# Kernel optimization log

Hardware: AMD Instinct MI355X
Metric: run time of the kernel (lower is better)

## Reference

```python
import jax, jax.numpy as jnp
import numpy as np

B, S, N, F, H, E = 1, 32, 2048, 64, 128, 32768


def setup_inputs() -> dict:
    key = jax.random.key(0)
    ks = jax.random.split(key, 13)
    p = lambda k, shp: (jax.random.normal(k, shp, dtype=jnp.float32) * 0.05)
    return {
        "x": jax.random.normal(ks[0], (B, S, N, F), dtype=jnp.float32),
        "edge_indexs": jax.random.randint(ks[1], (1, 2, S * E), 0, N, dtype=jnp.int64),
        "edgenum": E,
        "W1": p(ks[2], (F, H)), "b1": p(ks[3], (H,)),
        "W2": p(ks[4], (H, H)), "b2": p(ks[5], (H,)),
        "Wrel": p(ks[6], (H, H)), "brel": p(ks[7], (H,)),
        "Wroot": p(ks[8], (H, H)),
        "W3": p(ks[9], (H, H)), "b3": p(ks[10], (H,)),
        "W4": p(ks[11], (H, 1)), "b4": p(ks[12], (1,)),
    }


def reference(x, edge_indexs, edgenum, W1, b1, W2, b2, Wrel, brel, Wroot, W3, b3, W4, b4):
    batch, seq_len, num_stocks, _ = x.shape
    lrelu = jax.nn.leaky_relu  # default slope 0.01, matches nn.LeakyReLU()
    h = lrelu(x @ W1 + b1)
    h = lrelu(h @ W2 + b2)                       # [B,S,N,H]
    h = h.reshape(seq_len, num_stocks, -1)       # batch==1
    # split of [2, S*E] along edge dim into per-timestep graphs
    edges = edge_indexs[0].reshape(2, seq_len, edgenum)

    def step(h_t, src, tgt):
        # GraphConv(aggr='mean'): lin_rel(mean_j x_j) + lin_root(x_i)
        agg = jax.ops.segment_sum(h_t[src], tgt, num_segments=num_stocks)
        cnt = jax.ops.segment_sum(jnp.ones((edgenum,), h_t.dtype), tgt,
                                  num_segments=num_stocks)
        agg = agg / jnp.maximum(cnt, 1.0)[:, None]
        # all gnn layers share weights and each re-reads output[i], so one
        # application reproduces the original loop's final `out` exactly
        return lrelu(agg @ Wrel + brel + h_t @ Wroot)

    gnn_out = jax.vmap(step)(h, edges[0], edges[1])          # [S,N,H]
    out = gnn_out.reshape(batch, seq_len, num_stocks, -1)
    out = lrelu(out @ W3 + b3)
    out = out @ W4 + b4                                      # [B,S,N,1]
    return out[:, -1].reshape(batch, num_stocks, -1)
```

## Files before the change

kernel.cpp:

```cpp
#include <hip/hip_runtime.h>


#define N_NODES 2048
#define F_IN 64
#define H_DIM 128
#define S_LEN 32
#define E_EDGES 32768
#define T_LAST (S_LEN - 1)
#define CAP 96
#define NBLK 256
#define TPB 512

__device__ __forceinline__ float lrelu(float v) { return v > 0.0f ? v : 0.01f * v; }

__global__ __launch_bounds__(TPB) void k_fused(
    const float* __restrict__ x, const int* __restrict__ ei,
    const float* __restrict__ W1, const float* __restrict__ b1,
    const float* __restrict__ W2, const float* __restrict__ b2,
    const float* __restrict__ Wrel, const float* __restrict__ brel,
    const float* __restrict__ Wroot,
    const float* __restrict__ W3, const float* __restrict__ b3,
    const float* __restrict__ W4, const float* __restrict__ b4,
    float* __restrict__ out,
    int* __restrict__ deg, unsigned int* __restrict__ bar,
    int* __restrict__ bucket, float* __restrict__ h2)
{
    __shared__ float xs[8][F_IN];
    __shared__ float h1s[8][H_DIM];
    __shared__ float aggs[8][H_DIM];
    __shared__ float h2s[8][H_DIM];
    __shared__ float gs[8][H_DIM];
    __shared__ int   bl[8][CAP];
    __shared__ int   dgs[8];
    __shared__ float pred[8][2];

    const int t = threadIdx.x;
    const int bid = blockIdx.x;
    const int node0 = bid * 8;

    if (t < 128) {
        const int e = bid * 128 + t;
        const int src = ei[(size_t)T_LAST * E_EDGES + e];
        const int tgt = ei[(size_t)(S_LEN + T_LAST) * E_EDGES + e];
        const int slot = atomicAdd(&deg[tgt], 1);
        if (slot < CAP) bucket[tgt * CAP + slot] = src;
    }

    if (t < 256) {
        const float* xsrc = x + ((size_t)T_LAST * N_NODES + node0) * F_IN;
        ((float2*)&xs[0][0])[t] = ((const float2*)xsrc)[t];
    }
    __syncthreads();

    const int j = t & 127;
    const int q = t >> 7;
    const int nb = q * 2;

    {
        const float bb = b1[j];
        float a0 = bb, a1 = bb;
        for (int k = 0; k < F_IN; ++k) {
            const float w = W1[k * H_DIM + j];
            a0 += xs[nb][k] * w; a1 += xs[nb + 1][k] * w;
        }
        h1s[nb][j] = lrelu(a0); h1s[nb + 1][j] = lrelu(a1);
    }
    __syncthreads();
    {
        const float bb = b2[j];
        float a0 = bb, a1 = bb;
        for (int k = 0; k < H_DIM; ++k) {
            const float w = W2[k * H_DIM + j];
            a0 += h1s[nb][k] * w; a1 += h1s[nb + 1][k] * w;
        }
        a0 = lrelu(a0); a1 = lrelu(a1);
        h2[(size_t)(node0 + nb) * H_DIM + j] = a0;
        h2[(size_t)(node0 + nb + 1) * H_DIM + j] = a1;
        h2s[nb][j] = a0; h2s[nb + 1][j] = a1;
    }

    __syncthreads();
    if (t == 0) {
        __hip_atomic_fetch_add(bar, 1u, __ATOMIC_ACQ_REL, __HIP_MEMORY_SCOPE_AGENT);
        while (__hip_atomic_load(bar, __ATOMIC_ACQUIRE, __HIP_MEMORY_SCOPE_AGENT) < NBLK)
            __builtin_amdgcn_s_sleep(1);
    }
    __syncthreads();

    {
        const int g = t >> 6, lane = t & 63;
        const int n = node0 + g;
        const int dg = min(deg[n], CAP);
        if (lane == 0) dgs[g] = dg;
        for (int i = lane; i < dg; i += 64) bl[g][i] = bucket[n * CAP + i];
    }
    __syncthreads();

    #pragma unroll
    for (int m = 0; m < 2; ++m) {
        const int n = nb + m;
        const int dg = dgs[n];
        float acc = 0.0f;
        for (int i = 0; i < dg; ++i)
            acc += h2[(size_t)bl[n][i] * H_DIM + j];
        aggs[n][j] = acc / fmaxf((float)dg, 1.0f);
    }
    __syncthreads();

    {
        const float bb = brel[j];
        float a0 = bb, a1 = bb;
        for (int k = 0; k < H_DIM; ++k) {
            const float wr = Wrel[k * H_DIM + j];
            const float wo = Wroot[k * H_DIM + j];
            a0 += aggs[nb][k] * wr + h2s[nb][k] * wo;
            a1 += aggs[nb + 1][k] * wr + h2s[nb + 1][k] * wo;
        }
        gs[nb][j] = lrelu(a0); gs[nb + 1][j] = lrelu(a1);
    }
    __syncthreads();

    float p0, p1;
    {
        const float bb = b3[j];
        float a0 = bb, a1 = bb;
        for (int k = 0; k < H_DIM; ++k) {
            const float w = W3[k * H_DIM + j];
            a0 += gs[nb][k] * w; a1 += gs[nb + 1][k] * w;
        }
        const float w4 = W4[j];
        p0 = lrelu(a0) * w4; p1 = lrelu(a1) * w4;
    }
    for (int off = 32; off >= 1; off >>= 1) {
        p0 += __shfl_down(p0, off);
        p1 += __shfl_down(p1, off);
    }
    const int w = t >> 6;
    if ((t & 63) == 0) { pred[w][0] = p0; pred[w][1] = p1; }
    __syncthreads();
    if (t < 8) {
        const int n = t, qq = n >> 1, mm = n & 1;
        out[node0 + n] = pred[2 * qq][mm] + pred[2 * qq + 1][mm] + b4[0];
    }
}

extern "C" void kernel_launch(void* const* d_in, const int* in_sizes, int n_in,
                              void* d_out, int out_size, void* d_ws, size_t ws_size,
                              hipStream_t stream)
{
    const float* x     = (const float*)d_in[0];
    const int*   ei    = (const int*)d_in[1];
    const float* W1    = (const float*)d_in[3];
    const float* b1    = (const float*)d_in[4];
    const float* W2    = (const float*)d_in[5];
    const float* b2    = (const float*)d_in[6];
    const float* Wrel  = (const float*)d_in[7];
    const float* brel  = (const float*)d_in[8];
    const float* Wroot = (const float*)d_in[9];
    const float* W3    = (const float*)d_in[10];
    const float* b3    = (const float*)d_in[11];
    const float* W4    = (const float*)d_in[12];
    const float* b4    = (const float*)d_in[13];
    float* out = (float*)d_out;

    int*      deg    = (int*)d_ws;
    unsigned* bar    = (unsigned*)((int*)d_ws + 2048);
    int*      bucket = (int*)d_ws + 2064;
    float*    h2     = (float*)((int*)d_ws + 2064 + N_NODES * CAP);

    hipMemsetAsync(d_ws, 0, (2048 + 16) * sizeof(int), stream);

    k_fused<<<NBLK, TPB, 0, stream>>>(x, ei, W1, b1, W2, b2, Wrel, brel, Wroot,
                                      W3, b3, W4, b4, out, deg, bar, bucket, h2);
}
```

Baseline: 128.1 us.

## Split fused kernel at grid barrier into two launches with one node per thread-row

Replaces the software grid-wide spin barrier with a kernel boundary, splitting the fused kernel into an MLP/edge-bucketing kernel and a GNN aggregation/head kernel. Block size doubles to 1024 threads so each thread computes one node-feature output instead of two. The neighbour-gather loop is unrolled by four with independent accumulators to expose more memory parallelism. This trades the spin-wait for an extra launch and reloading h2 from global memory, and halves per-thread weight reuse.

After: 161.7 us. +26.2%, slower.

```diff
diff --git a/kernel.cpp b/kernel.cpp
--- a/kernel.cpp
+++ b/kernel.cpp
@@ -9,31 +9,18 @@
 #define T_LAST (S_LEN - 1)
 #define CAP 96
 #define NBLK 256
-#define TPB 512
+#define TPB 1024
 
 __device__ __forceinline__ float lrelu(float v) { return v > 0.0f ? v : 0.01f * v; }
 
-__global__ __launch_bounds__(TPB) void k_fused(
+__global__ __launch_bounds__(TPB) void kA(
     const float* __restrict__ x, const int* __restrict__ ei,
     const float* __restrict__ W1, const float* __restrict__ b1,
     const float* __restrict__ W2, const float* __restrict__ b2,
-    const float* __restrict__ Wrel, const float* __restrict__ brel,
-    const float* __restrict__ Wroot,
-    const float* __restrict__ W3, const float* __restrict__ b3,
-    const float* __restrict__ W4, const float* __restrict__ b4,
-    float* __restrict__ out,
-    int* __restrict__ deg, unsigned int* __restrict__ bar,
-    int* __restrict__ bucket, float* __restrict__ h2)
+    int* __restrict__ deg, int* __restrict__ bucket, float* __restrict__ h2)
 {
     __shared__ float xs[8][F_IN];
     __shared__ float h1s[8][H_DIM];
-    __shared__ float aggs[8][H_DIM];
-    __shared__ float h2s[8][H_DIM];
-    __shared__ float gs[8][H_DIM];
-    __shared__ int   bl[8][CAP];
-    __shared__ int   dgs[8];
-    __shared__ float pred[8][2];
-
     const int t = threadIdx.x;
     const int bid = blockIdx.x;
     const int node0 = bid * 8;
@@ -46,102 +33,82 @@
         if (slot < CAP) bucket[tgt * CAP + slot] = src;
     }
 
-    if (t < 256) {
-        const float* xsrc = x + ((size_t)T_LAST * N_NODES + node0) * F_IN;
-        ((float2*)&xs[0][0])[t] = ((const float2*)xsrc)[t];
-    }
+    if (t < 512)
+        ((float*)xs)[t] = x[((size_t)T_LAST * N_NODES + node0) * F_IN + t];
     __syncthreads();
 
+    const int n = t >> 7;
     const int j = t & 127;
-    const int q = t >> 7;
-    const int nb = q * 2;
 
-    {
-        const float bb = b1[j];
-        float a0 = bb, a1 = bb;
-        for (int k = 0; k < F_IN; ++k) {
-            const float w = W1[k * H_DIM + j];
-            a0 += xs[nb][k] * w; a1 += xs[nb + 1][k] * w;
-        }
-        h1s[nb][j] = lrelu(a0); h1s[nb + 1][j] = lrelu(a1);
-    }
-    __syncthreads();
-    {
-        const float bb = b2[j];
-        float a0 = bb, a1 = bb;
-        for (int k = 0; k < H_DIM; ++k) {
-            const float w = W2[k * H_DIM + j];
-            a0 += h1s[nb][k] * w; a1 += h1s[nb + 1][k] * w;
-        }
-        a0 = lrelu(a0); a1 = lrelu(a1);
-        h2[(size_t)(node0 + nb) * H_DIM + j] = a0;
-        h2[(size_t)(node0 + nb + 1) * H_DIM + j] = a1;
-        h2s[nb][j] = a0; h2s[nb + 1][j] = a1;
-    }
-
-    __syncthreads();
-    if (t == 0) {
-        __hip_atomic_fetch_add(bar, 1u, __ATOMIC_ACQ_REL, __HIP_MEMORY_SCOPE_AGENT);
-        while (__hip_atomic_load(bar, __ATOMIC_ACQUIRE, __HIP_MEMORY_SCOPE_AGENT) < NBLK)
-            __builtin_amdgcn_s_sleep(1);
-    }
+    float acc = b1[j];
+    #pragma unroll
+    for (int k = 0; k < F_IN; ++k)
+        acc += xs[n][k] * W1[k * H_DIM + j];
+    h1s[n][j] = lrelu(acc);
     __syncthreads();
 
-    {
-        const int g = t >> 6, lane = t & 63;
-        const int n = node0 + g;
-        const int dg = min(deg[n], CAP);
-        if (lane == 0) dgs[g] = dg;
-        for (int i = lane; i < dg; i += 64) bl[g][i] = bucket[n * CAP + i];
-    }
+    float a2 = b2[j];
+    #pragma unroll
+    for (int k = 0; k < H_DIM; ++k)
+        a2 += h1s[n][k] * W2[k * H_DIM + j];
+    h2[(size_t)(node0 + n) * H_DIM + j] = lrelu(a2);
+}
+
+__global__ __launch_bounds__(TPB) void kB(
+    const float* __restrict__ h2,
+    const int* __restrict__ deg, const int* __restrict__ bucket,
+    const float* __restrict__ Wrel, const float* __restrict__ brel,
+    const float* __restrict__ Wroot,
+    const float* __restrict__ W3, const float* __restrict__ b3,
+    const float* __restrict__ W4, const float* __restrict__ b4,
+    float* __restrict__ out)
+{
+    __shared__ float h2s[8][H_DIM];
+    __shared__ float aggs[8][H_DIM];
+    __shared__ float gs[8][H_DIM];
+    __shared__ int   bl[8][CAP];
+    __shared__ float pred[16];
+    const int t = threadIdx.x;
+    const int node0 = blockIdx.x * 8;
+    const int n = t >> 7;
+    const int j = t & 127;
+
+    h2s[n][j] = h2[(size_t)(node0 + n) * H_DIM + j];
+    const int dg = min(deg[node0 + n], CAP);
+    if (j < dg) bl[n][j] = bucket[(node0 + n) * CAP + j];
     __syncthreads();
 
-    #pragma unroll
-    for (int m = 0; m < 2; ++m) {
-        const int n = nb + m;
-        const int dg = dgs[n];
-        float acc = 0.0f;
-        for (int i = 0; i < dg; ++i)
-            acc += h2[(size_t)bl[n][i] * H_DIM + j];
-        aggs[n][j] = acc / fmaxf((float)dg, 1.0f);
+    float a0 = 0.f, a1 = 0.f, a2 = 0.f, a3 = 0.f;
+    int i = 0;
+    for (; i + 3 < dg; i += 4) {
+        const int s0 = bl[n][i], s1 = bl[n][i + 1], s2 = bl[n][i + 2], s3 = bl[n][i + 3];
+        a0 += h2[(size_t)s0 * H_DIM + j];
+        a1 += h2[(size_t)s1 * H_DIM + j];
+        a2 += h2[(size_t)s2 * H_DIM + j];
+        a3 += h2[(size_t)s3 * H_DIM + j];
     }
+    for (; i < dg; ++i) a0 += h2[(size_t)bl[n][i] * H_DIM + j];
+    aggs[n][j] = ((a0 + a1) + (a2 + a3)) / fmaxf((float)dg, 1.0f);
     __syncthreads();
 
-    {
-        const float bb = brel[j];
-        float a0 = bb, a1 = bb;
-        for (int k = 0; k < H_DIM; ++k) {
-            const float wr = Wrel[k * H_DIM + j];
-            const float wo = Wroot[k * H_DIM + j];
-            a0 += aggs[nb][k] * wr + h2s[nb][k] * wo;
-            a1 += aggs[nb + 1][k] * wr + h2s[nb + 1][k] * wo;
-        }
-        gs[nb][j] = lrelu(a0); gs[nb + 1][j] = lrelu(a1);
-    }
+    float g = brel[j];
+    #pragma unroll
+    for (int k = 0; k < H_DIM; ++k)
+        g += aggs[n][k] * Wrel[k * H_DIM + j] + h2s[n][k] * Wroot[k * H_DIM + j];
+    gs[n][j] = lrelu(g);
     __syncthreads();
 
-    float p0, p1;
-    {
-        const float bb = b3[j];
-        float a0 = bb, a1 = bb;
-        for (int k = 0; k < H_DIM; ++k) {
-            const float w = W3[k * H_DIM + j];
-            a0 += gs[nb][k] * w; a1 += gs[nb + 1][k] * w;
-        }
-        const float w4 = W4[j];
-        p0 = lrelu(a0) * w4; p1 = lrelu(a1) * w4;
-    }
-    for (int off = 32; off >= 1; off >>= 1) {
-        p0 += __shfl_down(p0, off);
-        p1 += __shfl_down(p1, off);
-    }
-    const int w = t >> 6;
-    if ((t & 63) == 0) { pred[w][0] = p0; pred[w][1] = p1; }
+    float h = b3[j];
+    #pragma unroll
+    for (int k = 0; k < H_DIM; ++k)
+        h += gs[n][k] * W3[k * H_DIM + j];
+    float p = lrelu(h) * W4[j];
+
+    for (int off = 32; off >= 1; off >>= 1) p += __shfl_down(p, off);
+    if ((t & 63) == 0) pred[t >> 6] = p;
     __syncthreads();
-    if (t < 8) {
-        const int n = t, qq = n >> 1, mm = n & 1;
-        out[node0 + n] = pred[2 * qq][mm] + pred[2 * qq + 1][mm] + b4[0];
-    }
+    if (t < 8)
+        out[node0 + t] = pred[2 * t] + pred[2 * t + 1] + b4[0];
 }
 
 extern "C" void kernel_launch(void* const* d_in, const int* in_sizes, int n_in,
@@ -163,13 +130,12 @@
     const float* b4    = (const float*)d_in[13];
     float* out = (float*)d_out;
 
-    int*      deg    = (int*)d_ws;
-    unsigned* bar    = (unsigned*)((int*)d_ws + 2048);
-    int*      bucket = (int*)d_ws + 2064;
-    float*    h2     = (float*)((int*)d_ws + 2064 + N_NODES * CAP);
+    int*   deg    = (int*)d_ws;
+    int*   bucket = deg + N_NODES;
+    float* h2     = (float*)(bucket + (size_t)N_NODES * CAP);
 
-    hipMemsetAsync(d_ws, 0, (2048 + 16) * sizeof(int), stream);
-
-    k_fused<<<NBLK, TPB, 0, stream>>>(x, ei, W1, b1, W2, b2, Wrel, brel, Wroot,
-                                      W3, b3, W4, b4, out, deg, bar, bucket, h2);
+    hipMemsetAsync(deg, 0, N_NODES * sizeof(int), stream);
+    kA<<<NBLK, TPB, 0, stream>>>(x, ei, W1, b1, W2, b2, deg, bucket, h2);
+    kB<<<NBLK, TPB, 0, stream>>>(h2, deg, bucket, Wrel, brel, Wroot,
+                                 W3, b3, W4, b4, out);
 }
```
